# Kernel optimization log

Hardware: AMD Instinct MI355X
Metric: run time of the kernel (lower is better)

The kernel has to match this reference:

```python
import jax, jax.numpy as jnp
import numpy as np

TARGET_H, TARGET_W = 602, 602
EPS = 1e-8
A = -0.75  # PyTorch bicubic kernel coefficient


def _cubic_kernel(x):
    # Keys cubic convolution kernel with a = -0.75 (PyTorch's choice), x >= 0
    x = np.abs(x)
    w = np.where(
        x <= 1.0,
        (A + 2.0) * x**3 - (A + 3.0) * x**2 + 1.0,
        np.where(x < 2.0, A * (x**3 - 5.0 * x**2 + 8.0 * x - 4.0), 0.0),
    )
    return w


def build_bicubic_matrix(in_size, out_size):
    # Row-stochastic [out_size, in_size] matrix equivalent to 1D bicubic resize
    # with align_corners=False and border replication (PyTorch F.interpolate).
    scale = in_size / out_size
    i = np.arange(out_size, dtype=np.float64)
    src = (i + 0.5) * scale - 0.5
    base = np.floor(src).astype(np.int64)
    t = src - base
    W = np.zeros((out_size, in_size), dtype=np.float64)
    for tap in range(-1, 3):
        idx = np.clip(base + tap, 0, in_size - 1)
        w = _cubic_kernel(t - tap)
        np.add.at(W, (np.arange(out_size), idx), w)
    return jnp.asarray(W, dtype=jnp.float32)


def setup_inputs() -> dict:
    key = jax.random.key(0)
    k1, k2 = jax.random.split(key)
    B, K, D, N = 4, 1849, 1024, 80
    feats = jax.random.normal(k1, (B, K, D), dtype=jnp.float32)
    embeddings = jax.random.normal(k2, (N, D), dtype=jnp.float32)
    return {"feats": feats, "embeddings": embeddings}


def reference(feats, embeddings) -> jnp.ndarray:
    B, K, D = feats.shape
    N = embeddings.shape[0]
    P = int(np.sqrt(K))  # patch grid side (43)

    # Cosine similarity ('init' branch with normalize=True), expressed as a GEMM
    dot = jnp.einsum("bkd,nd->bnk", feats, embeddings)  # [B,N,K]
    f_norm = jnp.linalg.norm(feats, axis=-1)       # [B,K]
    e_norm = jnp.linalg.norm(embeddings, axis=-1)  # [N]
    cosim = dot / (f_norm[:, None, :] * e_norm[None, :, None] + EPS)

    cosim = cosim.reshape(B, N, P, P)

    # Separable bicubic resize to (TARGET_H, TARGET_W)
    Wh = build_bicubic_matrix(P, TARGET_H)  # [602, P]
    Ww = build_bicubic_matrix(P, TARGET_W)  # [602, P]
    out = jnp.einsum("bnhw,Hh->bnHw", cosim, Wh)
    out = jnp.einsum("bnHw,Ww->bnHW", out, Ww)
    return out
```

## Files before the change

kernel.cpp:

```cpp
#include <hip/hip_runtime.h>
#include <math.h>

#define EPS 1e-8f
constexpr int D     = 1024;
constexpr int NEMB  = 80;
constexpr int K     = 1849;
constexpr int BATCH = 4;
constexpr int P     = 43;
constexpr int TGT   = 602;
constexpr int ROWS  = BATCH * K;
constexpr size_t PLANE = (size_t)BATCH * NEMB * K;
constexpr int SPLIT = 16;
constexpr int KC    = D / SPLIT;

typedef float nfloat4 __attribute__((ext_vector_type(4)));

__device__ inline double cubic_w(double x) {
  const double A = -0.75;
  x = fabs(x);
  if (x <= 1.0) return ((A + 2.0) * x - (A + 3.0)) * x * x + 1.0;
  if (x < 2.0)  return A * (((x - 5.0) * x + 8.0) * x - 4.0);
  return 0.0;
}

__device__ inline float block_reduce_sum256(float v) {
  #pragma unroll
  for (int off = 32; off > 0; off >>= 1) v += __shfl_down(v, off, 64);
  __shared__ float red[4];
  int lane = threadIdx.x & 63, wid = threadIdx.x >> 6;
  if (lane == 0) red[wid] = v;
  __syncthreads();
  float r = 0.f;
  if (threadIdx.x == 0) r = red[0] + red[1] + red[2] + red[3];
  return r;
}

__global__ __launch_bounds__(256) void prep_kernel(
    const float* __restrict__ emb, float* __restrict__ e_norm,
    float4* __restrict__ gtw) {
  int bid = blockIdx.x;
  if (bid < NEMB) {
    float4 v = ((const float4*)(emb + (size_t)bid * D))[threadIdx.x];
    float s = v.x * v.x + v.y * v.y + v.z * v.z + v.w * v.w;
    s = block_reduce_sum256(s);
    if (threadIdx.x == 0) e_norm[bid] = sqrtf(s);
  } else {
    int j = threadIdx.x;
    if (j < 14) {
      double scale = (double)P / (double)TGT;
      double src = ((double)j + 0.5) * scale - 0.5;
      double fb = floor(src);
      double t = src - fb;
      float4 w;
      w.x = (float)cubic_w(t + 1.0);
      w.y = (float)cubic_w(t);
      w.z = (float)cubic_w(t - 1.0);
      w.w = (float)cubic_w(t - 2.0);
      gtw[j] = w;
    }
  }
}

constexpr int BM  = 64;
constexpr int BK  = 32;
constexpr int LDA = 36;
constexpr int NT  = KC / BK;

__device__ inline float dot4(float4 v) {
  return v.x * v.x + v.y * v.y + v.z * v.z + v.w * v.w;
}

__global__ __launch_bounds__(256) void gemm_partial(
    const float* __restrict__ feats, const float* __restrict__ emb,
    float* __restrict__ part, float* __restrict__ fpart) {
  __shared__ float As[BM * LDA];
  __shared__ float Bs[NEMB * LDA];
  int t = threadIdx.x;
  int row0 = blockIdx.x * BM;
  int s = blockIdx.y;
  int tr = t >> 4, tc = t & 15;
  float acc[4][5] = {{0.f}};
  float ssq0 = 0.f, ssq1 = 0.f;

  int r = t >> 3, dg = t & 7;
  int gr0 = row0 + r, gr1 = row0 + 32 + r;
  bool ok0 = gr0 < ROWS, ok1 = gr1 < ROWS;
  const float* pA0 = feats + (size_t)gr0 * D + dg * 4;
  const float* pA1 = feats + (size_t)gr1 * D + dg * 4;
  const float* pB0 = emb + (size_t)r * D + dg * 4;
  const float* pB1 = emb + (size_t)(32 + r) * D + dg * 4;
  const float* pB2 = emb + (size_t)(64 + r) * D + dg * 4;
  bool okB2 = t < 128;

  int kbeg = s * KC;
  const float4 zero = make_float4(0.f, 0.f, 0.f, 0.f);
  float4 a0 = ok0 ? *(const float4*)(pA0 + kbeg) : zero;
  float4 a1 = ok1 ? *(const float4*)(pA1 + kbeg) : zero;
  float4 b0 = *(const float4*)(pB0 + kbeg);
  float4 b1 = *(const float4*)(pB1 + kbeg);
  float4 b2 = okB2 ? *(const float4*)(pB2 + kbeg) : zero;

  for (int tile = 0; tile < NT; ++tile) {
    ssq0 += dot4(a0);
    *(float4*)(As + r * LDA + dg * 4) = a0;
    ssq1 += dot4(a1);
    *(float4*)(As + (32 + r) * LDA + dg * 4) = a1;
    *(float4*)(Bs + r * LDA + dg * 4) = b0;
    *(float4*)(Bs + (32 + r) * LDA + dg * 4) = b1;
    if (okB2) *(float4*)(Bs + (64 + r) * LDA + dg * 4) = b2;
    __syncthreads();

    if (tile + 1 < NT) {
      int k1 = kbeg + (tile + 1) * BK;
      a0 = ok0 ? *(const float4*)(pA0 + k1) : zero;
      a1 = ok1 ? *(const float4*)(pA1 + k1) : zero;
      b0 = *(const float4*)(pB0 + k1);
      b1 = *(const float4*)(pB1 + k1);
      if (okB2) b2 = *(const float4*)(pB2 + k1);
    }

    #pragma unroll
    for (int dd = 0; dd < BK; dd += 4) {
      float4 a[4], b[5];
      #pragma unroll
      for (int j = 0; j < 4; ++j)  a[j]  = *(const float4*)(As + (tr * 4 + j) * LDA + dd);
      #pragma unroll
      for (int i2 = 0; i2 < 5; ++i2) b[i2] = *(const float4*)(Bs + (tc + i2 * 16) * LDA + dd);
      #pragma unroll
      for (int j = 0; j < 4; ++j)
        #pragma unroll
        for (int i2 = 0; i2 < 5; ++i2)
          acc[j][i2] += a[j].x * b[i2].x + a[j].y * b[i2].y +
                        a[j].z * b[i2].z + a[j].w * b[i2].w;
    }
    __syncthreads();
  }

  #pragma unroll
  for (int off = 4; off > 0; off >>= 1) {
    ssq0 += __shfl_down(ssq0, off, 8);
    ssq1 += __shfl_down(ssq1, off, 8);
  }
  if ((t & 7) == 0) {
    if (gr0 < ROWS) fpart[(size_t)s * ROWS + gr0] = ssq0;
    if (gr1 < ROWS) fpart[(size_t)s * ROWS + gr1] = ssq1;
  }

  float* pplane = part + (size_t)s * PLANE;
  #pragma unroll
  for (int j = 0; j < 4; ++j) {
    int gr = row0 + tr * 4 + j;
    if (gr >= ROWS) continue;
    int b_ = gr / K;
    int k  = gr - b_ * K;
    #pragma unroll
    for (int i2 = 0; i2 < 5; ++i2) {
      int n = tc + i2 * 16;
      pplane[((size_t)(b_ * NEMB + n)) * K + k] = acc[j][i2];
    }
  }
}

__global__ __launch_bounds__(256) void reduce_kernel(
    const float* __restrict__ part, const float* __restrict__ fpart,
    const float* __restrict__ e_norm, float* __restrict__ cosim) {
  size_t e = (size_t)blockIdx.x * 256 + threadIdx.x;
  if (e >= PLANE) return;
  int bn = (int)(e / K);
  int k  = (int)(e - (size_t)bn * K);
  int b_ = bn / NEMB;
  int n  = bn - b_ * NEMB;
  int gr = b_ * K + k;
  float dot = 0.f, fn2 = 0.f;
  #pragma unroll
  for (int s = 0; s < SPLIT; ++s) {
    dot += part[(size_t)s * PLANE + e];
    fn2 += fpart[(size_t)s * ROWS + gr];
  }
  cosim[e] = dot / (sqrtf(fn2) * e_norm[n] + EPS);
}

__global__ __launch_bounds__(320) void resize_kernel(
    const float* __restrict__ cosim, const float4* __restrict__ gtw,
    float* __restrict__ out) {
  __shared__ float img[5 * P];
  __shared__ float4 wq[14];
  __shared__ float obuf[14 * TGT];

  int bn = blockIdx.y;
  int c  = blockIdx.x;
  int t  = threadIdx.x;

  int hmin = max(0, c - 2), hmax = min(P - 1, c + 2);
  int NH = hmax - hmin + 1;

  if (t < 14) wq[t] = gtw[t];
  const float* src = cosim + (size_t)bn * (P * P) + hmin * P;
  for (int i = t; i < NH * P; i += 320) img[i] = src[i];
  __syncthreads();

  int pw = t;
  if (pw < TGT / 2) {
    int W0 = pw * 2;
    int m0 = W0 / 14;
    int j0 = W0 - m0 * 14;
    int wb0 = m0 - 2 + (j0 >= 7);
    int j1 = (j0 == 13) ? 0 : j0 + 1;
    int d  = (j0 == 6) ? 1 : 0;
    float4 w0 = wq[j0], w1 = wq[j1];

    int i0 = min(P - 1, max(0, wb0));
    int i1 = min(P - 1, max(0, wb0 + 1));
    int i2 = min(P - 1, max(0, wb0 + 2));
    int i3 = min(P - 1, max(0, wb0 + 3));
    int i4 = min(P - 1, max(0, wb0 + 4));

    float ta[5], tb[5];
    #pragma unroll
    for (int h = 0; h < 5; ++h) {
      const float* rowp = img + h * P;
      float v0 = rowp[i0], v1 = rowp[i1], v2 = rowp[i2], v3 = rowp[i3], v4 = rowp[i4];
      ta[h] = w0.x * v0 + w0.y * v1 + w0.z * v2 + w0.w * v3;
      float u0 = d ? v1 : v0;
      float u1 = d ? v2 : v1;
      float u2 = d ? v3 : v2;
      float u3 = d ? v4 : v3;
      tb[h] = w1.x * u0 + w1.y * u1 + w1.z * u2 + w1.w * u3;
    }

    #define ROWS7(R0, a0, a1, a2, a3)                                        \
      _Pragma("unroll")                                                      \
      for (int r = R0; r < R0 + 7; ++r) {                                    \
        float4 hw = wq[r];                                                   \
        float ox = hw.x * ta[a0] + hw.y * ta[a1] + hw.z * ta[a2] + hw.w * ta[a3]; \
        float oy = hw.x * tb[a0] + hw.y * tb[a1] + hw.z * tb[a2] + hw.w * tb[a3]; \
        *(float2*)(obuf + r * TGT + W0) = make_float2(ox, oy);               \
      }

    if (c >= 2 && c <= 40) {
      ROWS7(0, 0, 1, 2, 3)
      ROWS7(7, 1, 2, 3, 4)
    } else if (c == 0) {
      ROWS7(0, 0, 0, 0, 1)
      ROWS7(7, 0, 0, 1, 2)
    } else if (c == 1) {
      ROWS7(0, 0, 0, 1, 2)
      ROWS7(7, 0, 1, 2, 3)
    } else if (c == 41) {
      ROWS7(0, 0, 1, 2, 3)
      ROWS7(7, 1, 2, 3, 3)
    } else {
      ROWS7(0, 0, 1, 2, 2)
      ROWS7(7, 1, 2, 2, 2)
    }
    #undef ROWS7
  }
  __syncthreads();

  nfloat4* dst = (nfloat4*)(out + (size_t)bn * TGT * TGT + (size_t)c * 14 * TGT);
  const nfloat4* sb = (const nfloat4*)obuf;
  constexpr int NVEC = 14 * TGT / 4;
  for (int i = t; i < NVEC; i += 320) {
    __builtin_nontemporal_store(sb[i], dst + i);
  }
}

extern "C" void kernel_launch(void* const* d_in, const int* in_sizes, int n_in,
                              void* d_out, int out_size, void* d_ws, size_t ws_size,
                              hipStream_t stream) {
  const float* feats = (const float*)d_in[0];
  const float* emb   = (const float*)d_in[1];
  float* out = (float*)d_out;
  char* ws = (char*)d_ws;

  auto align64 = [](size_t x) { return (x + 63) & ~(size_t)63; };
  size_t off = 0;
  float* cosim  = (float*)(ws + off); off = align64(off + PLANE * 4);
  float* e_norm = (float*)(ws + off); off = align64(off + NEMB * 4);
  float4* gtw   = (float4*)(ws + off); off = align64(off + 14 * 16);
  float* fpart  = (float*)(ws + off); off = align64(off + (size_t)SPLIT * ROWS * 4);
  float* part   = (float*)(ws + off); off = align64(off + (size_t)SPLIT * PLANE * 4);

  prep_kernel<<<dim3(NEMB + 1), dim3(256), 0, stream>>>(emb, e_norm, gtw);
  gemm_partial<<<dim3((ROWS + BM - 1) / BM, SPLIT), dim3(256), 0, stream>>>(
      feats, emb, part, fpart);
  reduce_kernel<<<dim3((int)((PLANE + 255) / 256)), dim3(256), 0, stream>>>(
      part, fpart, e_norm, cosim);
  resize_kernel<<<dim3(43, 320), dim3(320), 0, stream>>>(cosim, gtw, out);
}
```

Baseline: 194.6 us.

## Write resize output directly from registers with 4-wide columns, halve GEMM K-split

The resize kernel no longer stages its 14x602 output tile in shared memory. Each of 150 threads computes four output columns and writes float4 nontemporal stores straight to global memory. Row alignment is handled by column parity, and two edge threads cover the leftover columns with float2 stores. This drops about 34 KB of LDS per block plus a barrier, which should raise occupancy, and the block size falls to 192 threads. The GEMM split-K also goes from 16 to 8, which shrinks the partial-sum buffer and the reduce traffic but gives the GEMM fewer blocks to run in parallel.

```diff
diff --git a/kernel.cpp b/kernel.cpp
--- a/kernel.cpp
+++ b/kernel.cpp
@@ -10,7 +10,7 @@
 constexpr int TGT   = 602;
 constexpr int ROWS  = BATCH * K;
 constexpr size_t PLANE = (size_t)BATCH * NEMB * K;
-constexpr int SPLIT = 16;
+constexpr int SPLIT = 8;
 constexpr int KC    = D / SPLIT;
 
 typedef float nfloat4 __attribute__((ext_vector_type(4)));
@@ -180,12 +180,11 @@
   cosim[e] = dot / (sqrtf(fn2) * e_norm[n] + EPS);
 }
 
-__global__ __launch_bounds__(320) void resize_kernel(
+__global__ __launch_bounds__(192) void resize_kernel(
     const float* __restrict__ cosim, const float4* __restrict__ gtw,
     float* __restrict__ out) {
   __shared__ float img[5 * P];
   __shared__ float4 wq[14];
-  __shared__ float obuf[14 * TGT];
 
   int bn = blockIdx.y;
   int c  = blockIdx.x;
@@ -196,72 +195,125 @@
 
   if (t < 14) wq[t] = gtw[t];
   const float* src = cosim + (size_t)bn * (P * P) + hmin * P;
-  for (int i = t; i < NH * P; i += 320) img[i] = src[i];
+  for (int i = t; i < NH * P; i += 192) img[i] = src[i];
   __syncthreads();
 
-  int pw = t;
-  if (pw < TGT / 2) {
-    int W0 = pw * 2;
+  float* obase = out + (size_t)bn * TGT * TGT + (size_t)(c * 14) * TGT;
+
+  if (t < 150) {
+    int W0 = t * 4;
+    int m0 = W0 / 14;
+    int j0 = W0 - m0 * 14;
+    int base0 = m0 - 2 + (j0 >= 7);
+
+    int s[6]; float4 w[6];
+    #pragma unroll
+    for (int i = 0; i < 6; ++i) {
+      int jj = j0 + i, mm = m0;
+      if (jj >= 14) { jj -= 14; mm += 1; }
+      w[i] = wq[jj];
+      s[i] = (mm - 2 + (jj >= 7)) - base0;
+    }
+    int ii[5];
+    #pragma unroll
+    for (int k = 0; k < 5; ++k) ii[k] = min(P - 1, max(0, base0 + k));
+
+    float ta[6][5];
+    #pragma unroll
+    for (int h = 0; h < 5; ++h) {
+      const float* rowp = img + h * P;
+      float v0 = rowp[ii[0]], v1 = rowp[ii[1]], v2 = rowp[ii[2]],
+            v3 = rowp[ii[3]], v4 = rowp[ii[4]];
+      #pragma unroll
+      for (int i = 0; i < 6; ++i) {
+        float u0 = s[i] ? v1 : v0;
+        float u1 = s[i] ? v2 : v1;
+        float u2 = s[i] ? v3 : v2;
+        float u3 = s[i] ? v4 : v3;
+        ta[i][h] = w[i].x * u0 + w[i].y * u1 + w[i].z * u2 + w[i].w * u3;
+      }
+    }
+
+    #define VROWS(R0, a0, a1, a2, a3)                                          \
+      _Pragma("unroll")                                                        \
+      for (int r = R0; r < R0 + 7; ++r) {                                      \
+        float4 hw = wq[r];                                                     \
+        const int co = (r & 1) ? 2 : 0;                                        \
+        nfloat4 o;                                                             \
+        o.x = hw.x*ta[co+0][a0] + hw.y*ta[co+0][a1] + hw.z*ta[co+0][a2] + hw.w*ta[co+0][a3]; \
+        o.y = hw.x*ta[co+1][a0] + hw.y*ta[co+1][a1] + hw.z*ta[co+1][a2] + hw.w*ta[co+1][a3]; \
+        o.z = hw.x*ta[co+2][a0] + hw.y*ta[co+2][a1] + hw.z*ta[co+2][a2] + hw.w*ta[co+2][a3]; \
+        o.w = hw.x*ta[co+3][a0] + hw.y*ta[co+3][a1] + hw.z*ta[co+3][a2] + hw.w*ta[co+3][a3]; \
+        __builtin_nontemporal_store(o, (nfloat4*)(obase + (size_t)r * TGT + W0 + co)); \
+      }
+
+    if (c >= 2 && c <= 40) {
+      VROWS(0, 0, 1, 2, 3)
+      VROWS(7, 1, 2, 3, 4)
+    } else if (c == 0) {
+      VROWS(0, 0, 0, 0, 1)
+      VROWS(7, 0, 0, 1, 2)
+    } else if (c == 1) {
+      VROWS(0, 0, 0, 1, 2)
+      VROWS(7, 0, 1, 2, 3)
+    } else if (c == 41) {
+      VROWS(0, 0, 1, 2, 3)
+      VROWS(7, 1, 2, 3, 3)
+    } else {
+      VROWS(0, 0, 1, 2, 2)
+      VROWS(7, 1, 2, 2, 2)
+    }
+    #undef VROWS
+  } else if (t < 152) {
+    int W0 = (t == 150) ? 600 : 0;
+    int par = (t == 150) ? 0 : 1;
     int m0 = W0 / 14;
     int j0 = W0 - m0 * 14;
     int wb0 = m0 - 2 + (j0 >= 7);
-    int j1 = (j0 == 13) ? 0 : j0 + 1;
-    int d  = (j0 == 6) ? 1 : 0;
-    float4 w0 = wq[j0], w1 = wq[j1];
+    float4 w0 = wq[j0], w1 = wq[j0 + 1];
 
     int i0 = min(P - 1, max(0, wb0));
     int i1 = min(P - 1, max(0, wb0 + 1));
     int i2 = min(P - 1, max(0, wb0 + 2));
     int i3 = min(P - 1, max(0, wb0 + 3));
-    int i4 = min(P - 1, max(0, wb0 + 4));
 
     float ta[5], tb[5];
     #pragma unroll
     for (int h = 0; h < 5; ++h) {
       const float* rowp = img + h * P;
-      float v0 = rowp[i0], v1 = rowp[i1], v2 = rowp[i2], v3 = rowp[i3], v4 = rowp[i4];
+      float v0 = rowp[i0], v1 = rowp[i1], v2 = rowp[i2], v3 = rowp[i3];
       ta[h] = w0.x * v0 + w0.y * v1 + w0.z * v2 + w0.w * v3;
-      float u0 = d ? v1 : v0;
-      float u1 = d ? v2 : v1;
-      float u2 = d ? v3 : v2;
-      float u3 = d ? v4 : v3;
-      tb[h] = w1.x * u0 + w1.y * u1 + w1.z * u2 + w1.w * u3;
-    }
-
-    #define ROWS7(R0, a0, a1, a2, a3)                                        \
-      _Pragma("unroll")                                                      \
-      for (int r = R0; r < R0 + 7; ++r) {                                    \
-        float4 hw = wq[r];                                                   \
-        float ox = hw.x * ta[a0] + hw.y * ta[a1] + hw.z * ta[a2] + hw.w * ta[a3]; \
-        float oy = hw.x * tb[a0] + hw.y * tb[a1] + hw.z * tb[a2] + hw.w * tb[a3]; \
-        *(float2*)(obuf + r * TGT + W0) = make_float2(ox, oy);               \
+      tb[h] = w1.x * v0 + w1.y * v1 + w1.z * v2 + w1.w * v3;
+    }
+
+    #define TROWS(R0, a0, a1, a2, a3)                                          \
+      _Pragma("unroll")                                                        \
+      for (int r = R0; r < R0 + 7; ++r) {                                      \
+        if ((r & 1) == par) {                                                  \
+          float4 hw = wq[r];                                                   \
+          float ox = hw.x*ta[a0] + hw.y*ta[a1] + hw.z*ta[a2] + hw.w*ta[a3];    \
+          float oy = hw.x*tb[a0] + hw.y*tb[a1] + hw.z*tb[a2] + hw.w*tb[a3];    \
+          *(float2*)(obase + (size_t)r * TGT + W0) = make_float2(ox, oy);      \
+        }                                                                      \
       }
 
     if (c >= 2 && c <= 40) {
-      ROWS7(0, 0, 1, 2, 3)
-      ROWS7(7, 1, 2, 3, 4)
+      TROWS(0, 0, 1, 2, 3)
+      TROWS(7, 1, 2, 3, 4)
     } else if (c == 0) {
-      ROWS7(0, 0, 0, 0, 1)
-      ROWS7(7, 0, 0, 1, 2)
+      TROWS(0, 0, 0, 0, 1)
+      TROWS(7, 0, 0, 1, 2)
     } else if (c == 1) {
-      ROWS7(0, 0, 0, 1, 2)
-      ROWS7(7, 0, 1, 2, 3)
+      TROWS(0, 0, 0, 1, 2)
+      TROWS(7, 0, 1, 2, 3)
     } else if (c == 41) {
-      ROWS7(0, 0, 1, 2, 3)
-      ROWS7(7, 1, 2, 3, 3)
+      TROWS(0, 0, 1, 2, 3)
+      TROWS(7, 1, 2, 3, 3)
     } else {
-      ROWS7(0, 0, 1, 2, 2)
-      ROWS7(7, 1, 2, 2, 2)
-    }
-    #undef ROWS7
-  }
-  __syncthreads();
-
-  nfloat4* dst = (nfloat4*)(out + (size_t)bn * TGT * TGT + (size_t)c * 14 * TGT);
-  const nfloat4* sb = (const nfloat4*)obuf;
-  constexpr int NVEC = 14 * TGT / 4;
-  for (int i = t; i < NVEC; i += 320) {
-    __builtin_nontemporal_store(sb[i], dst + i);
+      TROWS(0, 0, 1, 2, 2)
+      TROWS(7, 1, 2, 2, 2)
+    }
+    #undef TROWS
   }
 }
 
@@ -286,5 +338,5 @@
       feats, emb, part, fpart);
   reduce_kernel<<<dim3((int)((PLANE + 255) / 256)), dim3(256), 0, stream>>>(
       part, fpart, e_norm, cosim);
-  resize_kernel<<<dim3(43, 320), dim3(320), 0, stream>>>(cosim, gtw, out);
-}
+  resize_kernel<<<dim3(43, 320), dim3(192), 0, stream>>>(cosim, gtw, out);
+}
```

Measured after the change: 203.7 us. 4.7% more time.
